# Optimization experiments

Measured on AMD Instinct MI355X. Metric: run time of the kernel, lower is better.

## Reference

```python
import jax, jax.numpy as jnp
import numpy as np

T, B, I, H = 256, 128, 1024, 1024


def setup_inputs() -> dict:
    key = jax.random.key(0)
    ks = jax.random.split(key, 5)
    s = 1.0 / np.sqrt(H)  # PyTorch GRU init scale
    return {
        "x": jax.random.normal(ks[0], (T, B, I), dtype=jnp.float32),
        "w_ih": jax.random.uniform(ks[1], (3 * H, I), jnp.float32, -s, s),
        "w_hh": jax.random.uniform(ks[2], (3 * H, H), jnp.float32, -s, s),
        "b_ih": jax.random.uniform(ks[3], (3 * H,), jnp.float32, -s, s),
        "b_hh": jax.random.uniform(ks[4], (3 * H,), jnp.float32, -s, s),
    }


def reference(x, w_ih, w_hh, b_ih, b_hh):
    # Single-layer GRU over full sequence, h0 = zeros (matches init_hidden).
    # PyTorch gate order in the 3H dim: reset (r), update (z), new (n).
    h_dim = w_hh.shape[1]
    batch = x.shape[1]
    # Precompute all input projections in one big GEMM: [T,B,3H]
    xg = jnp.einsum("tbi,gi->tbg", x, w_ih) + b_ih

    def step(h, xg_t):
        hg = h @ w_hh.T + b_hh  # [B,3H]
        xr, xz, xn = jnp.split(xg_t, 3, axis=-1)
        hr, hz, hn = jnp.split(hg, 3, axis=-1)
        r = jax.nn.sigmoid(xr + hr)
        z = jax.nn.sigmoid(xz + hz)
        n = jnp.tanh(xn + r * hn)
        h_new = (1.0 - z) * n + z * h
        return h_new, h_new

    h0 = jnp.zeros((batch, h_dim), dtype=x.dtype)
    _, outs = jax.lax.scan(step, h0, xg)  # outs: [T,B,H]
    return outs
```

## Files before the change

kernel.cpp:

```cpp
#include <hip/hip_runtime.h>
#include <hip/hip_bf16.h>
#include <cstdint>
#include <cstddef>


typedef __attribute__((ext_vector_type(4))) float f32x4;
typedef __attribute__((ext_vector_type(8))) short s16x8;
typedef __attribute__((ext_vector_type(4))) unsigned short u16x4;

static __device__ __forceinline__ unsigned short f2bf(float f) {
  union { float f; unsigned u; } v; v.f = f;
  unsigned u = v.u;
  u += 0x7FFFu + ((u >> 16) & 1u);
  return (unsigned short)(u >> 16);
}
static __device__ __forceinline__ float bf2f(unsigned short h) {
  union { unsigned u; float f; } v; v.u = ((unsigned)h) << 16;
  return v.f;
}
static __device__ __forceinline__ float sigm(float x) {
  float e = __builtin_amdgcn_exp2f(-1.442695041f * x);
  return __builtin_amdgcn_rcpf(1.f + e);
}
static __device__ __forceinline__ float tanh_f(float x) {
  float e = __builtin_amdgcn_exp2f(2.885390082f * x);
  return 1.f - 2.f * __builtin_amdgcn_rcpf(e + 1.f);
}

static __device__ __forceinline__ s16x8 ld16_l2(const unsigned short* p) {
  s16x8 r;
  asm volatile("global_load_dwordx4 %0, %1, off sc0" : "=v"(r) : "v"(p) : "memory");
  return r;
}
static __device__ __forceinline__ void st2_l2(unsigned short* p, unsigned short v) {
  unsigned vv = v;
  asm volatile("global_store_short %0, %1, off sc0" :: "v"(p), "v"(vv) : "memory");
}
static __device__ __forceinline__ s16x8 ld16_mall(const unsigned short* p) {
  s16x8 r;
  asm volatile("global_load_dwordx4 %0, %1, off sc0 sc1" : "=v"(r) : "v"(p) : "memory");
  return r;
}
static __device__ __forceinline__ void st2_mall(unsigned short* p, unsigned short v) {
  unsigned vv = v;
  asm volatile("global_store_short %0, %1, off sc0 sc1" :: "v"(p), "v"(vv) : "memory");
}
static __device__ __forceinline__ void st_flag(unsigned int* p, unsigned v) {
  asm volatile("global_store_dword %0, %1, off sc0 sc1" :: "v"(p), "v"(v) : "memory");
}
static __device__ __forceinline__ unsigned ld_flag(const unsigned int* p) {
  unsigned r;
  asm volatile("global_load_dword %0, %1, off sc0 sc1\n\ts_waitcnt vmcnt(0)"
               : "=v"(r) : "v"(p) : "memory");
  return r;
}
static __device__ __forceinline__ void add1_l2(unsigned int* p) {
  asm volatile("global_atomic_add %0, %1, off" :: "v"(p), "v"(1u) : "memory");
}
static __device__ __forceinline__ void add1_mall(unsigned int* p) {
  asm volatile("global_atomic_add %0, %1, off sc1" :: "v"(p), "v"(1u) : "memory");
}
static __device__ __forceinline__ unsigned poll_l2(unsigned int* p) {
  unsigned old;
  asm volatile("global_atomic_add %0, %1, %2, off sc0\n\ts_waitcnt vmcnt(0)"
               : "=v"(old) : "v"(p), "v"(0u) : "memory");
  return old;
}
static __device__ __forceinline__ unsigned poll_mall(unsigned int* p) {
  unsigned old;
  asm volatile("global_atomic_add %0, %1, %2, off sc0 sc1\n\ts_waitcnt vmcnt(0)"
               : "=v"(old) : "v"(p), "v"(0u) : "memory");
  return old;
}

__global__ __launch_bounds__(256)
void cvt_bf16(const float* __restrict__ src, unsigned short* __restrict__ dst, int n4) {
  int i = blockIdx.x * 256 + threadIdx.x;
  int stride = gridDim.x * 256;
  for (; i < n4; i += stride) {
    f32x4 v = ((const f32x4*)src)[i];
    u16x4 o = { f2bf(v.x), f2bf(v.y), f2bf(v.z), f2bf(v.w) };
    ((u16x4*)dst)[i] = o;
  }
}

__global__ __launch_bounds__(512, 1)
void gru_scan(const unsigned short* __restrict__ xbf,
              const float* __restrict__ Whh,
              const float* __restrict__ Wih,
              const float* __restrict__ bhh,
              const float* __restrict__ bih,
              float* __restrict__ out,
              unsigned short* __restrict__ hbc,
              unsigned int* __restrict__ bar)
{
  __shared__ char hbuf[32768];
  __shared__ char xbuf[32768];
  __shared__ float part[8][4][64][4];
  __shared__ int fastsh;

  const int tid = threadIdx.x;
  const int lane = tid & 63;
  const int wv = tid >> 6;
  const int id = blockIdx.x;
  const int bg = id & 7;
  const int cg = id >> 3;
  const int c0 = cg * 32;
  const int b0 = bg * 16;
  const int r16 = lane & 15, r4 = lane >> 4;
  const int ks = wv >> 1, nt = wv & 1;

  unsigned int* cnt = bar + bg * 32;
  unsigned int* dflags = bar + 8192 + bg * 32;

  unsigned myxcc = (__builtin_amdgcn_s_getreg(63508) & 0xFu) | 0x100u;
  if (tid == 0) st_flag(dflags + cg, myxcc);
  if (wv == 0) {
    unsigned v;
    for (;;) {
      v = ld_flag(dflags + (lane & 31));
      if (__ballot(v < 0x100u) == 0) break;
      __builtin_amdgcn_s_sleep(1);
    }
    int bad = (v != myxcc);
    if (tid == 0) fastsh = (__ballot(bad) == 0) ? 1 : 0;
  }
  __syncthreads();
  const bool fast = (fastsh != 0);

  s16x8 bwh[3][8], bwi[3][8];
  #pragma unroll
  for (int n = 0; n < 3; ++n) {
    const float* hrow = Whh + (size_t)(n * 1024 + c0 + nt * 16 + r16) * 1024;
    const float* irow = Wih + (size_t)(n * 1024 + c0 + nt * 16 + r16) * 1024;
    #pragma unroll
    for (int kc = 0; kc < 8; ++kc) {
      int k = ks * 256 + kc * 32 + r4 * 8;
      f32x4 h0 = *(const f32x4*)(hrow + k);
      f32x4 h1 = *(const f32x4*)(hrow + k + 4);
      f32x4 i0 = *(const f32x4*)(irow + k);
      f32x4 i1 = *(const f32x4*)(irow + k + 4);
      s16x8 fh, fi;
      fh[0] = (short)f2bf(h0.x); fh[1] = (short)f2bf(h0.y);
      fh[2] = (short)f2bf(h0.z); fh[3] = (short)f2bf(h0.w);
      fh[4] = (short)f2bf(h1.x); fh[5] = (short)f2bf(h1.y);
      fh[6] = (short)f2bf(h1.z); fh[7] = (short)f2bf(h1.w);
      fi[0] = (short)f2bf(i0.x); fi[1] = (short)f2bf(i0.y);
      fi[2] = (short)f2bf(i0.z); fi[3] = (short)f2bf(i0.w);
      fi[4] = (short)f2bf(i1.x); fi[5] = (short)f2bf(i1.y);
      fi[6] = (short)f2bf(i1.z); fi[7] = (short)f2bf(i1.w);
      bwh[n][kc] = fh;
      bwi[n][kc] = fi;
    }
  }

  const int grow = tid >> 5;
  const int gcolL = tid & 31;
  const int gcol = c0 + gcolL;
  const int g_nt = gcolL >> 4, g_c16 = gcolL & 15;
  const int g_lane = (grow >> 2) * 16 + g_c16;
  const int g_rg = grow & 3;
  const float bR  = bhh[gcol] + bih[gcol];
  const float bZ  = bhh[1024 + gcol] + bih[1024 + gcol];
  const float bNh = bhh[2048 + gcol];
  const float bNx = bih[2048 + gcol];
  float hprev = 0.f;

  const int arow = lane & 15;
  const int aswz = (arow & 7) << 4;
  const int abase = arow * 2048;
  const int g16 = (lane >> 4) * 16;

  const int scb = nt * 1024 + lane * 16;
  int s_goff[4], s_loff[4];
  #pragma unroll
  for (int i = 0; i < 4; ++i) {
    int row = i * 4 + ks;
    s_goff[i] = (b0 + row) * 1024 + (scb >> 1);
    s_loff[i] = row * 2048 + (scb ^ ((row & 7) << 4));
  }

  #pragma unroll
  for (int i = 0; i < 4; ++i)
    *(f32x4*)(hbuf + tid * 64 + i * 16) = (f32x4){0.f, 0.f, 0.f, 0.f};
  {
    s16x8 v0 = *(const s16x8*)(xbf + s_goff[0]);
    s16x8 v1 = *(const s16x8*)(xbf + s_goff[1]);
    s16x8 v2 = *(const s16x8*)(xbf + s_goff[2]);
    s16x8 v3 = *(const s16x8*)(xbf + s_goff[3]);
    *(s16x8*)(xbuf + s_loff[0]) = v0;
    *(s16x8*)(xbuf + s_loff[1]) = v1;
    *(s16x8*)(xbuf + s_loff[2]) = v2;
    *(s16x8*)(xbuf + s_loff[3]) = v3;
  }
  __syncthreads();

  for (int t = 0; t < 256; ++t) {
    f32x4 aR = {0.f,0.f,0.f,0.f}, aZ = aR, aNh = aR, aNx = aR;
    #pragma unroll
    for (int kc = 0; kc < 8; ++kc) {
      int off = (ks * 512 + kc * 64 + g16) ^ aswz;
      s16x8 ah = *(const s16x8*)(hbuf + abase + off);
      s16x8 ax = *(const s16x8*)(xbuf + abase + off);
      aR  = __builtin_amdgcn_mfma_f32_16x16x32_bf16(ah, bwh[0][kc], aR, 0, 0, 0);
      aR  = __builtin_amdgcn_mfma_f32_16x16x32_bf16(ax, bwi[0][kc], aR, 0, 0, 0);
      aZ  = __builtin_amdgcn_mfma_f32_16x16x32_bf16(ah, bwh[1][kc], aZ, 0, 0, 0);
      aZ  = __builtin_amdgcn_mfma_f32_16x16x32_bf16(ax, bwi[1][kc], aZ, 0, 0, 0);
      aNh = __builtin_amdgcn_mfma_f32_16x16x32_bf16(ah, bwh[2][kc], aNh, 0, 0, 0);
      aNx = __builtin_amdgcn_mfma_f32_16x16x32_bf16(ax, bwi[2][kc], aNx, 0, 0, 0);
    }
    *(f32x4*)&part[wv][0][lane][0] = aR;
    *(f32x4*)&part[wv][1][lane][0] = aZ;
    *(f32x4*)&part[wv][2][lane][0] = aNh;
    *(f32x4*)&part[wv][3][lane][0] = aNx;
    __syncthreads();

    {
      float sr = bR, sz = bZ, snh = bNh, snx = bNx;
      #pragma unroll
      for (int kx = 0; kx < 4; ++kx) {
        sr  += part[kx * 2 + g_nt][0][g_lane][g_rg];
        sz  += part[kx * 2 + g_nt][1][g_lane][g_rg];
        snh += part[kx * 2 + g_nt][2][g_lane][g_rg];
        snx += part[kx * 2 + g_nt][3][g_lane][g_rg];
      }
      float rg = sigm(sr);
      float zg = sigm(sz);
      float ng = tanh_f(snx + rg * snh);
      float h = (1.f - zg) * ng + zg * hprev;
      hprev = h;
      unsigned short* wH = hbc + (size_t)((t + 1) & 1) * 131072;
      size_t widx = (size_t)(b0 + grow) * 1024 + gcol;
      if (fast) st2_l2(wH + widx, f2bf(h));
      else      st2_mall(wH + widx, f2bf(h));
      out[(size_t)t * 131072 + widx] = h;
      asm volatile("s_waitcnt vmcnt(1)" ::: "memory");
    }
    __syncthreads();

    if (tid == 0) {
      if (fast) add1_l2(cnt);
      else      add1_mall(cnt);
    }

    if (t < 255) {
      size_t xb = (size_t)(t + 1) * 131072;
      s16x8 x0 = *(const s16x8*)(xbf + xb + s_goff[0]);
      s16x8 x1 = *(const s16x8*)(xbf + xb + s_goff[1]);
      s16x8 x2 = *(const s16x8*)(xbf + xb + s_goff[2]);
      s16x8 x3 = *(const s16x8*)(xbf + xb + s_goff[3]);

      if (wv == 7 && lane == 0) {
        unsigned tgt = 32u * (unsigned)(t + 1);
        if (fast) {
          while (poll_l2(cnt) < tgt) {}
        } else {
          while (poll_mall(cnt) < tgt) __builtin_amdgcn_s_sleep(1);
        }
      }
      *(s16x8*)(xbuf + s_loff[0]) = x0;
      *(s16x8*)(xbuf + s_loff[1]) = x1;
      *(s16x8*)(xbuf + s_loff[2]) = x2;
      *(s16x8*)(xbuf + s_loff[3]) = x3;
      __syncthreads();

      const unsigned short* hs = hbc + (size_t)((t + 1) & 1) * 131072;
      s16x8 v0, v1, v2, v3;
      if (fast) {
        v0 = ld16_l2(hs + s_goff[0]); v1 = ld16_l2(hs + s_goff[1]);
        v2 = ld16_l2(hs + s_goff[2]); v3 = ld16_l2(hs + s_goff[3]);
      } else {
        v0 = ld16_mall(hs + s_goff[0]); v1 = ld16_mall(hs + s_goff[1]);
        v2 = ld16_mall(hs + s_goff[2]); v3 = ld16_mall(hs + s_goff[3]);
      }
      asm volatile("s_waitcnt vmcnt(0)" ::: "memory");
      *(s16x8*)(hbuf + s_loff[0]) = v0;
      *(s16x8*)(hbuf + s_loff[1]) = v1;
      *(s16x8*)(hbuf + s_loff[2]) = v2;
      *(s16x8*)(hbuf + s_loff[3]) = v3;
      __syncthreads();
    }
  }
}

extern "C" void kernel_launch(void* const* d_in, const int* in_sizes, int n_in,
                              void* d_out, int out_size, void* d_ws, size_t ws_size,
                              hipStream_t stream) {
  const float* x   = (const float*)d_in[0];
  const float* wih = (const float*)d_in[1];
  const float* whh = (const float*)d_in[2];
  const float* bih = (const float*)d_in[3];
  const float* bhh = (const float*)d_in[4];
  float* out = (float*)d_out;

  char* ws = (char*)d_ws;
  unsigned short* xbf = (unsigned short*)ws;
  unsigned short* hbc = (unsigned short*)(ws + 67108864);
  unsigned int*   bar = (unsigned int*)(ws + 67633152);

  hipMemsetAsync(bar, 0, 40960, stream);
  cvt_bf16<<<2048, 256, 0, stream>>>(x, xbf, 32768 * 1024 / 4);
  gru_scan<<<256, 512, 0, stream>>>(xbf, whh, wih, bhh, bih, out, hbc, bar);
}
```

Baseline: 853.2 us.

## Store x and h in MFMA fragment layout and split barrier per K-slice

```diff
diff --git a/kernel.cpp b/kernel.cpp
--- a/kernel.cpp
+++ b/kernel.cpp
@@ -14,10 +14,6 @@
   u += 0x7FFFu + ((u >> 16) & 1u);
   return (unsigned short)(u >> 16);
 }
-static __device__ __forceinline__ float bf2f(unsigned short h) {
-  union { unsigned u; float f; } v; v.u = ((unsigned)h) << 16;
-  return v.f;
-}
 static __device__ __forceinline__ float sigm(float x) {
   float e = __builtin_amdgcn_exp2f(-1.442695041f * x);
   return __builtin_amdgcn_rcpf(1.f + e);
@@ -74,18 +70,35 @@
 }
 
 __global__ __launch_bounds__(256)
-void cvt_bf16(const float* __restrict__ src, unsigned short* __restrict__ dst, int n4) {
-  int i = blockIdx.x * 256 + threadIdx.x;
+void cvt_xfrag(const float* __restrict__ src, unsigned short* __restrict__ dst) {
+  const int total = 32768 * 1024 / 8;
+  int G = blockIdx.x * 256 + threadIdx.x;
   int stride = gridDim.x * 256;
-  for (; i < n4; i += stride) {
-    f32x4 v = ((const f32x4*)src)[i];
-    u16x4 o = { f2bf(v.x), f2bf(v.y), f2bf(v.z), f2bf(v.w) };
-    ((u16x4*)dst)[i] = o;
+  for (; G < total; G += stride) {
+    int t  = G >> 14;
+    int r  = G & 16383;
+    int bg = r >> 11;
+    int q  = r & 2047;
+    int ks = q >> 9;
+    int w  = q & 511;
+    int kc = w >> 6;
+    int l  = w & 63;
+    int row = bg * 16 + (l & 15);
+    int col = ks * 256 + kc * 32 + (l >> 4) * 8;
+    const float* s = src + ((size_t)(t * 128 + row)) * 1024 + col;
+    f32x4 a = *(const f32x4*)(s);
+    f32x4 b = *(const f32x4*)(s + 4);
+    s16x8 o;
+    o[0] = (short)f2bf(a.x); o[1] = (short)f2bf(a.y);
+    o[2] = (short)f2bf(a.z); o[3] = (short)f2bf(a.w);
+    o[4] = (short)f2bf(b.x); o[5] = (short)f2bf(b.y);
+    o[6] = (short)f2bf(b.z); o[7] = (short)f2bf(b.w);
+    *(s16x8*)(dst + (size_t)G * 8) = o;
   }
 }
 
 __global__ __launch_bounds__(512, 1)
-void gru_scan(const unsigned short* __restrict__ xbf,
+void gru_scan(const unsigned short* __restrict__ xfrag,
               const float* __restrict__ Whh,
               const float* __restrict__ Wih,
               const float* __restrict__ bhh,
@@ -94,8 +107,6 @@
               unsigned short* __restrict__ hbc,
               unsigned int* __restrict__ bar)
 {
-  __shared__ char hbuf[32768];
-  __shared__ char xbuf[32768];
   __shared__ float part[8][4][64][4];
   __shared__ int fastsh;
 
@@ -110,7 +121,8 @@
   const int r16 = lane & 15, r4 = lane >> 4;
   const int ks = wv >> 1, nt = wv & 1;
 
-  unsigned int* cnt = bar + bg * 32;
+  unsigned int* qcnt  = bar + (size_t)(bg * 4 + ks) * 32;
+  unsigned int* mycnt = bar + (size_t)(bg * 4 + (cg >> 3)) * 32;
   unsigned int* dflags = bar + 8192 + bg * 32;
 
   unsigned myxcc = (__builtin_amdgcn_s_getreg(63508) & 0xFu) | 0x100u;
@@ -166,49 +178,75 @@
   const float bNx = bih[2048 + gcol];
   float hprev = 0.f;
 
-  const int arow = lane & 15;
-  const int aswz = (arow & 7) << 4;
-  const int abase = arow * 2048;
-  const int g16 = (lane >> 4) * 16;
-
-  const int scb = nt * 1024 + lane * 16;
-  int s_goff[4], s_loff[4];
-  #pragma unroll
-  for (int i = 0; i < 4; ++i) {
-    int row = i * 4 + ks;
-    s_goff[i] = (b0 + row) * 1024 + (scb >> 1);
-    s_loff[i] = row * 2048 + (scb ^ ((row & 7) << 4));
-  }
-
-  #pragma unroll
-  for (int i = 0; i < 4; ++i)
-    *(f32x4*)(hbuf + tid * 64 + i * 16) = (f32x4){0.f, 0.f, 0.f, 0.f};
-  {
-    s16x8 v0 = *(const s16x8*)(xbf + s_goff[0]);
-    s16x8 v1 = *(const s16x8*)(xbf + s_goff[1]);
-    s16x8 v2 = *(const s16x8*)(xbf + s_goff[2]);
-    s16x8 v3 = *(const s16x8*)(xbf + s_goff[3]);
-    *(s16x8*)(xbuf + s_loff[0]) = v0;
-    *(s16x8*)(xbuf + s_loff[1]) = v1;
-    *(s16x8*)(xbuf + s_loff[2]) = v2;
-    *(s16x8*)(xbuf + s_loff[3]) = v3;
-  }
-  __syncthreads();
+  const int p_ks = gcol >> 8;
+  const int p_kc = (gcol >> 5) & 7;
+  const int p_e5 = gcol & 31;
+  const int p_l  = ((p_e5 >> 3) << 4) | grow;
+  const size_t p_idx = (size_t)bg * 16384 + (size_t)p_ks * 4096 + p_kc * 512
+                     + p_l * 8 + (p_e5 & 7);
+
+  const size_t fbase = (size_t)bg * 16384 + (size_t)ks * 4096 + (size_t)lane * 8;
 
   for (int t = 0; t < 256; ++t) {
+    const unsigned short* xs = xfrag + (size_t)t * 131072 + fbase;
+    s16x8 ax[8];
+    #pragma unroll
+    for (int kc = 0; kc < 8; ++kc)
+      ax[kc] = *(const s16x8*)(xs + kc * 512);
+
     f32x4 aR = {0.f,0.f,0.f,0.f}, aZ = aR, aNh = aR, aNx = aR;
-    #pragma unroll
-    for (int kc = 0; kc < 8; ++kc) {
-      int off = (ks * 512 + kc * 64 + g16) ^ aswz;
-      s16x8 ah = *(const s16x8*)(hbuf + abase + off);
-      s16x8 ax = *(const s16x8*)(xbuf + abase + off);
-      aR  = __builtin_amdgcn_mfma_f32_16x16x32_bf16(ah, bwh[0][kc], aR, 0, 0, 0);
-      aR  = __builtin_amdgcn_mfma_f32_16x16x32_bf16(ax, bwi[0][kc], aR, 0, 0, 0);
-      aZ  = __builtin_amdgcn_mfma_f32_16x16x32_bf16(ah, bwh[1][kc], aZ, 0, 0, 0);
-      aZ  = __builtin_amdgcn_mfma_f32_16x16x32_bf16(ax, bwi[1][kc], aZ, 0, 0, 0);
-      aNh = __builtin_amdgcn_mfma_f32_16x16x32_bf16(ah, bwh[2][kc], aNh, 0, 0, 0);
-      aNx = __builtin_amdgcn_mfma_f32_16x16x32_bf16(ax, bwi[2][kc], aNx, 0, 0, 0);
-    }
+
+    if (t > 0) {
+      unsigned tgt = 8u * (unsigned)t;
+      if (fast) {
+        for (;;) {
+          unsigned v = 0;
+          if (lane == 0) v = poll_l2(qcnt);
+          v = __shfl(v, 0);
+          if (v >= tgt) break;
+        }
+      } else {
+        for (;;) {
+          unsigned v = 0;
+          if (lane == 0) v = poll_mall(qcnt);
+          v = __shfl(v, 0);
+          if (v >= tgt) break;
+          __builtin_amdgcn_s_sleep(1);
+        }
+      }
+
+      const unsigned short* hs = hbc + (size_t)(t & 1) * 131072 + fbase;
+      s16x8 ah[8];
+      if (fast) {
+        #pragma unroll
+        for (int kc = 0; kc < 8; ++kc)
+          ah[kc] = ld16_l2(hs + kc * 512);
+      } else {
+        #pragma unroll
+        for (int kc = 0; kc < 8; ++kc)
+          ah[kc] = ld16_mall(hs + kc * 512);
+      }
+      asm volatile("s_waitcnt vmcnt(0)" ::: "memory");
+      __builtin_amdgcn_sched_barrier(0);
+
+      #pragma unroll
+      for (int kc = 0; kc < 8; ++kc) {
+        aR  = __builtin_amdgcn_mfma_f32_16x16x32_bf16(ah[kc], bwh[0][kc], aR, 0, 0, 0);
+        aR  = __builtin_amdgcn_mfma_f32_16x16x32_bf16(ax[kc], bwi[0][kc], aR, 0, 0, 0);
+        aZ  = __builtin_amdgcn_mfma_f32_16x16x32_bf16(ah[kc], bwh[1][kc], aZ, 0, 0, 0);
+        aZ  = __builtin_amdgcn_mfma_f32_16x16x32_bf16(ax[kc], bwi[1][kc], aZ, 0, 0, 0);
+        aNh = __builtin_amdgcn_mfma_f32_16x16x32_bf16(ah[kc], bwh[2][kc], aNh, 0, 0, 0);
+        aNx = __builtin_amdgcn_mfma_f32_16x16x32_bf16(ax[kc], bwi[2][kc], aNx, 0, 0, 0);
+      }
+    } else {
+      #pragma unroll
+      for (int kc = 0; kc < 8; ++kc) {
+        aR  = __builtin_amdgcn_mfma_f32_16x16x32_bf16(ax[kc], bwi[0][kc], aR, 0, 0, 0);
+        aZ  = __builtin_amdgcn_mfma_f32_16x16x32_bf16(ax[kc], bwi[1][kc], aZ, 0, 0, 0);
+        aNx = __builtin_amdgcn_mfma_f32_16x16x32_bf16(ax[kc], bwi[2][kc], aNx, 0, 0, 0);
+      }
+    }
+
     *(f32x4*)&part[wv][0][lane][0] = aR;
     *(f32x4*)&part[wv][1][lane][0] = aZ;
     *(f32x4*)&part[wv][2][lane][0] = aNh;
@@ -229,56 +267,18 @@
       float ng = tanh_f(snx + rg * snh);
       float h = (1.f - zg) * ng + zg * hprev;
       hprev = h;
+      unsigned short hv = f2bf(h);
       unsigned short* wH = hbc + (size_t)((t + 1) & 1) * 131072;
-      size_t widx = (size_t)(b0 + grow) * 1024 + gcol;
-      if (fast) st2_l2(wH + widx, f2bf(h));
-      else      st2_mall(wH + widx, f2bf(h));
-      out[(size_t)t * 131072 + widx] = h;
+      if (fast) st2_l2(wH + p_idx, hv);
+      else      st2_mall(wH + p_idx, hv);
+      out[(size_t)t * 131072 + (size_t)(b0 + grow) * 1024 + gcol] = h;
       asm volatile("s_waitcnt vmcnt(1)" ::: "memory");
     }
     __syncthreads();
 
     if (tid == 0) {
-      if (fast) add1_l2(cnt);
-      else      add1_mall(cnt);
-    }
-
-    if (t < 255) {
-      size_t xb = (size_t)(t + 1) * 131072;
-      s16x8 x0 = *(const s16x8*)(xbf + xb + s_goff[0]);
-      s16x8 x1 = *(const s16x8*)(xbf + xb + s_goff[1]);
-      s16x8 x2 = *(const s16x8*)(xbf + xb + s_goff[2]);
-      s16x8 x3 = *(const s16x8*)(xbf + xb + s_goff[3]);
-
-      if (wv == 7 && lane == 0) {
-        unsigned tgt = 32u * (unsigned)(t + 1);
-        if (fast) {
-          while (poll_l2(cnt) < tgt) {}
-        } else {
-          while (poll_mall(cnt) < tgt) __builtin_amdgcn_s_sleep(1);
-        }
-      }
-      *(s16x8*)(xbuf + s_loff[0]) = x0;
-      *(s16x8*)(xbuf + s_loff[1]) = x1;
-      *(s16x8*)(xbuf + s_loff[2]) = x2;
-      *(s16x8*)(xbuf + s_loff[3]) = x3;
-      __syncthreads();
-
-      const unsigned short* hs = hbc + (size_t)((t + 1) & 1) * 131072;
-      s16x8 v0, v1, v2, v3;
-      if (fast) {
-        v0 = ld16_l2(hs + s_goff[0]); v1 = ld16_l2(hs + s_goff[1]);
-        v2 = ld16_l2(hs + s_goff[2]); v3 = ld16_l2(hs + s_goff[3]);
-      } else {
-        v0 = ld16_mall(hs + s_goff[0]); v1 = ld16_mall(hs + s_goff[1]);
-        v2 = ld16_mall(hs + s_goff[2]); v3 = ld16_mall(hs + s_goff[3]);
-      }
-      asm volatile("s_waitcnt vmcnt(0)" ::: "memory");
-      *(s16x8*)(hbuf + s_loff[0]) = v0;
-      *(s16x8*)(hbuf + s_loff[1]) = v1;
-      *(s16x8*)(hbuf + s_loff[2]) = v2;
-      *(s16x8*)(hbuf + s_loff[3]) = v3;
-      __syncthreads();
+      if (fast) add1_l2(mycnt);
+      else      add1_mall(mycnt);
     }
   }
 }
@@ -294,11 +294,11 @@
   float* out = (float*)d_out;
 
   char* ws = (char*)d_ws;
-  unsigned short* xbf = (unsigned short*)ws;
-  unsigned short* hbc = (unsigned short*)(ws + 67108864);
-  unsigned int*   bar = (unsigned int*)(ws + 67633152);
+  unsigned short* xfrag = (unsigned short*)ws;
+  unsigned short* hbc   = (unsigned short*)(ws + 67108864);
+  unsigned int*   bar   = (unsigned int*)(ws + 67633152);
 
   hipMemsetAsync(bar, 0, 40960, stream);
-  cvt_bf16<<<2048, 256, 0, stream>>>(x, xbf, 32768 * 1024 / 4);
-  gru_scan<<<256, 512, 0, stream>>>(xbf, whh, wih, bhh, bih, out, hbc, bar);
-}
+  cvt_xfrag<<<2048, 256, 0, stream>>>(x, xfrag);
+  gru_scan<<<256, 512, 0, stream>>>(xfrag, whh, wih, bhh, bih, out, hbc, bar);
+}
```

Measured after the change: 1.687 ms. 1.98x slower.
